# Performance work log

Measured on AMD Instinct MI355X. Metric: run time of the kernel, lower is better.

Reference implementation:

```python
import jax, jax.numpy as jnp
import numpy as np

EPS = 1e-5  # torch BatchNorm default


def setup_inputs() -> dict:
    key = jax.random.key(0)
    ks = jax.random.split(key, 8)
    B, Q, S, C = 4, 256, 128, 256
    feats = [2 * C, 256, 64, 1]  # opt['num_features']
    inp = {
        "support_features": jax.random.normal(ks[0], (B, S, C), dtype=jnp.float32),
        "query_features": jax.random.normal(ks[1], (B, Q, C), dtype=jnp.float32),
    }
    for i in range(3):
        fan_in, fan_out = feats[i], feats[i + 1]
        std = np.sqrt(2.0 / (fan_in + fan_out))  # xavier_normal on conv weight
        inp[f"W{i}"] = jax.random.normal(ks[2 + i], (fan_out, fan_in), dtype=jnp.float32) * std
        inp[f"b{i}"] = jnp.zeros((fan_out,), dtype=jnp.float32)
        inp[f"g{i}"] = jnp.ones((fan_out,), dtype=jnp.float32)   # BN weight
        inp[f"bt{i}"] = jnp.zeros((fan_out,), dtype=jnp.float32)  # BN bias
    return inp


def _bn_relu(x, g, bt):
    # x: [B, N, C]; BatchNorm1d training-mode stats over batch and length dims
    mean = jnp.mean(x, axis=(0, 1))
    var = jnp.mean(jnp.square(x - mean), axis=(0, 1))  # biased var, as torch BN
    return jax.nn.relu((x - mean) * (g * jax.lax.rsqrt(var + EPS)) + bt)


def reference(support_features, query_features,
              W0, b0, g0, bt0, W1, b1, g1, bt1, W2, b2, g2, bt2):
    B, S, C = support_features.shape
    Q = query_features.shape[1]
    # pairwise concat: [B, Q, S, 2C]
    uq = jnp.broadcast_to(query_features[:, :, None, :], (B, Q, S, C))
    us = jnp.broadcast_to(support_features[:, None, :, :], (B, Q, S, C))
    x = jnp.concatenate([uq, us], axis=3).reshape(B, Q * S, 2 * C)
    # 1x1 conv == matmul over channel dim
    x = _bn_relu(jnp.einsum('bnc,oc->bno', x, W0) + b0, g0, bt0)
    x = _bn_relu(jnp.einsum('bnc,oc->bno', x, W1) + b1, g1, bt1)
    x = _bn_relu(jnp.einsum('bnc,oc->bno', x, W2) + b2, g2, bt2)
    # back to [B, C_out, Q, S]
    return jnp.transpose(x, (0, 2, 1)).reshape(B, -1, Q, S)
```

## Files before the change

kernel.cpp:

```cpp
#include <hip/hip_runtime.h>
#include <hip/hip_bf16.h>


typedef __attribute__((ext_vector_type(4))) float f32x4;
typedef __attribute__((ext_vector_type(8))) short s16x8;

#define BN_EPS 1e-5f
#define INV_N  (1.0f/131072.0f)

#define LEAFA(g)   ((g)*16)
#define ROOTA      512
#define GATEA(g)   (528 + (g)*16)
#define CNT_ZERO   1040

__device__ __forceinline__ unsigned pk_bf16(float a, float b) {
  float2 t; t.x = a; t.y = b;
  __hip_bfloat162 h = __float22bfloat162_rn(t);
  return *reinterpret_cast<unsigned*>(&h);
}
__device__ __forceinline__ void split2(float a, float b, unsigned& uh, unsigned& ul) {
  uh = pk_bf16(a, b);
  float ha = __uint_as_float(uh << 16);
  float hb = __uint_as_float(uh & 0xFFFF0000u);
  ul = pk_bf16(a - ha, b - hb);
}

__device__ __forceinline__ unsigned a_ld(const unsigned* p) {
  return __hip_atomic_load(p, __ATOMIC_RELAXED, __HIP_MEMORY_SCOPE_AGENT);
}
__device__ __forceinline__ float a_ldf(const float* p) {
  return __hip_atomic_load(p, __ATOMIC_RELAXED, __HIP_MEMORY_SCOPE_AGENT);
}
__device__ __forceinline__ void a_st(unsigned* p, unsigned v) {
  __hip_atomic_store(p, v, __ATOMIC_RELAXED, __HIP_MEMORY_SCOPE_AGENT);
}
__device__ __forceinline__ void a_stf(float* p, float v) {
  __hip_atomic_store(p, v, __ATOMIC_RELAXED, __HIP_MEMORY_SCOPE_AGENT);
}
__device__ __forceinline__ unsigned a_add(unsigned* p) {
  return __hip_atomic_fetch_add(p, 1u, __ATOMIC_RELAXED, __HIP_MEMORY_SCOPE_AGENT);
}

union frag_u { s16x8 v; unsigned u[4]; };

struct Args {
  const float *Sf, *Qf, *W0, *b0, *g0, *bt0, *W1, *b1, *g1, *bt1, *W2, *b2, *g2, *bt2;
  float *Aq, *As, *y2, *ws0s, *ws1p, *ws1g, *ws1r, *ws2p, *out;
  unsigned *cnt;
};

__global__ __launch_bounds__(64) void k_g0(Args a)
{
  int bi = blockIdx.x, t = threadIdx.x;
  if (bi == 384) {
    for (int i = t; i < CNT_ZERO; i += 64) a.cnt[i] = 0u;
    return;
  }
  int l15 = t & 15, quad = t >> 4;
  int chunk = bi >> 2, ntile = bi & 3;
  bool isQ = (chunk < 64);
  const float* X; float* Out; int m0, koff;
  if (isQ) { m0 = chunk * 16; X = a.Qf; Out = a.Aq; koff = 0; }
  else     { m0 = (chunk - 64) * 16; X = a.Sf; Out = a.As; koff = 256; }
  int n0 = ntile * 64;

  f32x4 acc[4] = {};
#pragma unroll
  for (int ko = 0; ko < 256; ko += 32) {
    const float* row = X + (m0 + l15) * 256 + ko + quad * 8;
    f32x4 v0 = *(const f32x4*)(row);
    f32x4 v1 = *(const f32x4*)(row + 4);
    frag_u ah, al;
#pragma unroll
    for (int j = 0; j < 2; j++) {
      split2(v0[2 * j], v0[2 * j + 1], ah.u[j], al.u[j]);
      split2(v1[2 * j], v1[2 * j + 1], ah.u[2 + j], al.u[2 + j]);
    }
#pragma unroll
    for (int nt = 0; nt < 4; nt++) {
      const float* wrow = a.W0 + (n0 + nt * 16 + l15) * 512 + koff + ko + quad * 8;
      f32x4 w0v = *(const f32x4*)(wrow);
      f32x4 w1v = *(const f32x4*)(wrow + 4);
      frag_u bh, bl;
      split2(w0v[0], w0v[1], bh.u[0], bl.u[0]);
      split2(w0v[2], w0v[3], bh.u[1], bl.u[1]);
      split2(w1v[0], w1v[1], bh.u[2], bl.u[2]);
      split2(w1v[2], w1v[3], bh.u[3], bl.u[3]);
      acc[nt] = __builtin_amdgcn_mfma_f32_16x16x32_bf16(ah.v, bh.v, acc[nt], 0, 0, 0);
      acc[nt] = __builtin_amdgcn_mfma_f32_16x16x32_bf16(al.v, bh.v, acc[nt], 0, 0, 0);
      acc[nt] = __builtin_amdgcn_mfma_f32_16x16x32_bf16(ah.v, bl.v, acc[nt], 0, 0, 0);
    }
  }
#pragma unroll
  for (int nt = 0; nt < 4; nt++) {
    int o = n0 + nt * 16 + l15;
    float bias = isQ ? 0.0f : a.b0[o];
    float cs = 0, cs2 = 0;
#pragma unroll
    for (int r = 0; r < 4; r++) {
      float y = acc[nt][r] + bias;
      Out[(m0 + quad * 4 + r) * 256 + o] = y;
      cs += y; cs2 += y * y;
    }
    cs  += __shfl_xor(cs, 16);  cs  += __shfl_xor(cs, 32);
    cs2 += __shfl_xor(cs2, 16); cs2 += __shfl_xor(cs2, 32);
    if (quad == 0) {
      a.ws0s[chunk * 512 + o] = cs;
      a.ws0s[chunk * 512 + 256 + o] = cs2;
    }
  }
}

__device__ __forceinline__ void bn0_finalize(const Args& a, int t, float* sh_a0c0)
{
  int o = t;
  float sumY = 0, cross = 0, SQ2 = 0, SS2 = 0;
#pragma unroll
  for (int b = 0; b < 4; b++) {
    float sq1 = 0, sq2 = 0, ss1 = 0, ss2 = 0;
#pragma unroll
    for (int c = 0; c < 16; c++) {
      sq1 += a.ws0s[(b * 16 + c) * 512 + o];
      sq2 += a.ws0s[(b * 16 + c) * 512 + 256 + o];
    }
#pragma unroll
    for (int c = 0; c < 8; c++) {
      ss1 += a.ws0s[(64 + b * 8 + c) * 512 + o];
      ss2 += a.ws0s[(64 + b * 8 + c) * 512 + 256 + o];
    }
    SQ2 += sq2; SS2 += ss2;
    sumY += 128.0f * sq1 + 256.0f * ss1;
    cross += sq1 * ss1;
  }
  float mean = sumY * INV_N;
  float var = (128.0f * SQ2 + 256.0f * SS2 + 2.0f * cross) * INV_N - mean * mean;
  float aa = a.g0[o] * rsqrtf(var + BN_EPS);
  sh_a0c0[o] = aa;
  sh_a0c0[256 + o] = a.bt0[o] - mean * aa;
}

__global__ __launch_bounds__(256, 2) void k_f(Args a)
{
  int bi = blockIdx.x, t = threadIdx.x;
  int w = t >> 6, l = t & 63, l15 = l & 15, quad = l >> 4;
  __shared__ ushort w1f[2048 * 8];
  __shared__ float sh_a0c0[512];
  __shared__ float red[2][4][4][16];
  __shared__ float sh_tot[128];
  __shared__ float sh_a1c1[128];
  __shared__ float rs[16], rs2[16];
  __shared__ int s_role;

#pragma unroll
  for (int i = 0; i < 8; i++) {
    int fr = i * 256 + t;
    int kk = fr >> 8, r = fr & 255, nt = r >> 6, ln = r & 63;
    const float* src = a.W1 + (nt * 16 + (ln & 15)) * 256 + kk * 32 + (ln >> 4) * 8;
    f32x4 v0 = *(const f32x4*)(src);
    f32x4 v1 = *(const f32x4*)(src + 4);
    frag_u z;
    z.u[0] = pk_bf16(v0[0], v0[1]); z.u[1] = pk_bf16(v0[2], v0[3]);
    z.u[2] = pk_bf16(v1[0], v1[1]); z.u[3] = pk_bf16(v1[2], v1[3]);
    *(s16x8*)(w1f + fr * 8) = z.v;
  }
  bn0_finalize(a, t, sh_a0c0);
  __syncthreads();

  int b_ = bi >> 7, rem = bi & 127, qt = rem >> 3, st = rem & 7;
  const float* asrow = a.As + ((b_ << 7) + st * 16 + l15) * 256;
  const float* aqrow[4];
#pragma unroll
  for (int mt = 0; mt < 4; mt++)
    aqrow[mt] = a.Aq + ((b_ << 8) + qt * 16 + w * 4 + mt) * 256;

  f32x4 acc[4][4] = {};
#pragma unroll
  for (int kk = 0; kk < 8; kk++) {
    int obase = kk * 32 + quad * 8;
    f32x4 a0v0 = *(const f32x4*)(sh_a0c0 + obase);
    f32x4 a0v1 = *(const f32x4*)(sh_a0c0 + obase + 4);
    f32x4 c0v0 = *(const f32x4*)(sh_a0c0 + 256 + obase);
    f32x4 c0v1 = *(const f32x4*)(sh_a0c0 + 256 + obase + 4);
    f32x4 as0 = *(const f32x4*)(asrow + obase);
    f32x4 as1 = *(const f32x4*)(asrow + obase + 4);

    s16x8 zh[4];
#pragma unroll
    for (int mt = 0; mt < 4; mt++) {
      f32x4 aq0 = *(const f32x4*)(aqrow[mt] + obase);
      f32x4 aq1 = *(const f32x4*)(aqrow[mt] + obase + 4);
      f32x4 z0 = (aq0 + as0) * a0v0 + c0v0;
      f32x4 z1 = (aq1 + as1) * a0v1 + c0v1;
      frag_u zz;
      zz.u[0] = pk_bf16(fmaxf(z0[0], 0.0f), fmaxf(z0[1], 0.0f));
      zz.u[1] = pk_bf16(fmaxf(z0[2], 0.0f), fmaxf(z0[3], 0.0f));
      zz.u[2] = pk_bf16(fmaxf(z1[0], 0.0f), fmaxf(z1[1], 0.0f));
      zz.u[3] = pk_bf16(fmaxf(z1[2], 0.0f), fmaxf(z1[3], 0.0f));
      zh[mt] = zz.v;
    }
#pragma unroll
    for (int nt = 0; nt < 4; nt++) {
      s16x8 bw = *(const s16x8*)(w1f + ((kk * 4 + nt) * 64 + l) * 8);
#pragma unroll
      for (int mt = 0; mt < 4; mt++)
        acc[mt][nt] = __builtin_amdgcn_mfma_f32_16x16x32_bf16(zh[mt], bw, acc[mt][nt], 0, 0, 0);
    }
  }

  float biasv[4];
#pragma unroll
  for (int nt = 0; nt < 4; nt++) biasv[nt] = a.b1[nt * 16 + l15];
  unsigned ku01[4][4], ku23[4][4];
  float s[4] = {0, 0, 0, 0}, s2[4] = {0, 0, 0, 0};
#pragma unroll
  for (int mt = 0; mt < 4; mt++) {
#pragma unroll
    for (int nt = 0; nt < 4; nt++) {
      float y0 = acc[mt][nt][0] + biasv[nt];
      float y1 = acc[mt][nt][1] + biasv[nt];
      float y2v = acc[mt][nt][2] + biasv[nt];
      float y3 = acc[mt][nt][3] + biasv[nt];
      unsigned u01 = pk_bf16(y0, y1), u23 = pk_bf16(y2v, y3);
      ku01[mt][nt] = u01; ku23[mt][nt] = u23;
      float f0 = __uint_as_float(u01 << 16), f1 = __uint_as_float(u01 & 0xFFFF0000u);
      float f2 = __uint_as_float(u23 << 16), f3 = __uint_as_float(u23 & 0xFFFF0000u);
      s[nt]  += f0 + f1 + f2 + f3;
      s2[nt] += f0 * f0 + f1 * f1 + f2 * f2 + f3 * f3;
    }
  }
#pragma unroll
  for (int nt = 0; nt < 4; nt++) {
    float v = s[nt], v2 = s2[nt];
    v  += __shfl_xor(v, 16);  v  += __shfl_xor(v, 32);
    v2 += __shfl_xor(v2, 16); v2 += __shfl_xor(v2, 32);
    if (quad == 0) { red[0][w][nt][l15] = v; red[1][w][nt][l15] = v2; }
  }
  __syncthreads();
  if (t < 128) {
    int which = t >> 6, j = t & 63, nt = j >> 4, jl = j & 15;
    float v = red[which][0][nt][jl] + red[which][1][nt][jl] +
              red[which][2][nt][jl] + red[which][3][nt][jl];
    a_stf(&a.ws1p[bi * 128 + t], v);
  }

  asm volatile("s_waitcnt vmcnt(0)" ::: "memory");
  __syncthreads();
  int g = bi & 31;
  if (t == 0) {
    unsigned old = a_add(&a.cnt[LEAFA(g)]);
    s_role = (old == 15u) ? 1 : 0;
  }
  __syncthreads();
  if (s_role) {
    if (t < 128) {
      float sum = 0;
#pragma unroll
      for (int c = 0; c < 16; c++)
        sum += a_ldf(&a.ws1p[(g + c * 32) * 128 + t]);
      a_stf(&a.ws1g[g * 128 + t], sum);
    }
    asm volatile("s_waitcnt vmcnt(0)" ::: "memory");
    __syncthreads();
    if (t == 0) {
      unsigned r = a_add(&a.cnt[ROOTA]);
      s_role = (r == 31u) ? 2 : 1;
    }
    __syncthreads();
    if (s_role == 2) {
      if (t < 128) {
        float tot = 0;
#pragma unroll
        for (int gg = 0; gg < 32; gg++)
          tot += a_ldf(&a.ws1g[gg * 128 + t]);
        sh_tot[t] = tot;
      }
      __syncthreads();
      if (t < 64) {
        float mean = sh_tot[t] * INV_N;
        float var = sh_tot[64 + t] * INV_N - mean * mean;
        float aa = a.g1[t] * rsqrtf(var + BN_EPS);
        sh_a1c1[t] = aa;
        sh_a1c1[64 + t] = a.bt1[t] - mean * aa;
      }
      __syncthreads();
      if (t < 128) {
        float uv = sh_a1c1[t];
#pragma unroll
        for (int r2 = 0; r2 < 32; r2++)
          a_stf(&a.ws1r[r2 * 128 + t], uv);
      }
      asm volatile("s_waitcnt vmcnt(0)" ::: "memory");
      __syncthreads();
      if (t == 0) {
#pragma unroll
        for (int i = 0; i < 32; i++) a_st(&a.cnt[GATEA(i)], 1u);
      }
    }
  }
  if (t == 0) {
    while (a_ld(&a.cnt[GATEA(g)]) == 0u) __builtin_amdgcn_s_sleep(32);
  }
  __syncthreads();
  if (t < 128)
    sh_a1c1[t] = a_ldf(&a.ws1r[g * 128 + t]);
  __syncthreads();

  float a1v[4], c1v[4], w2v[4];
#pragma unroll
  for (int nt = 0; nt < 4; nt++) {
    int j = nt * 16 + l15;
    a1v[nt] = sh_a1c1[j]; c1v[nt] = sh_a1c1[64 + j]; w2v[nt] = a.W2[j];
  }
  float b2v = a.b2[0];
  float ls = 0, ls2 = 0;
#pragma unroll
  for (int mt = 0; mt < 4; mt++) {
    float part[4] = {0, 0, 0, 0};
#pragma unroll
    for (int nt = 0; nt < 4; nt++) {
      unsigned u01 = ku01[mt][nt], u23 = ku23[mt][nt];
      float f0 = __uint_as_float(u01 << 16), f1 = __uint_as_float(u01 & 0xFFFF0000u);
      float f2 = __uint_as_float(u23 << 16), f3 = __uint_as_float(u23 & 0xFFFF0000u);
      part[0] += fmaxf(a1v[nt] * f0 + c1v[nt], 0.0f) * w2v[nt];
      part[1] += fmaxf(a1v[nt] * f1 + c1v[nt], 0.0f) * w2v[nt];
      part[2] += fmaxf(a1v[nt] * f2 + c1v[nt], 0.0f) * w2v[nt];
      part[3] += fmaxf(a1v[nt] * f3 + c1v[nt], 0.0f) * w2v[nt];
    }
    f32x4 o;
#pragma unroll
    for (int r = 0; r < 4; r++) {
      float pv = part[r];
      pv += __shfl_xor(pv, 1); pv += __shfl_xor(pv, 2);
      pv += __shfl_xor(pv, 4); pv += __shfl_xor(pv, 8);
      float y = pv + b2v;
      o[r] = y;
      if (l15 == 0) { ls += y; ls2 += y * y; }
    }
    if (l15 == 0) {
      int q = qt * 16 + w * 4 + mt;
      int P = ((b_ * 256 + q) * 128) + st * 16 + quad * 4;
      *(f32x4*)(a.y2 + P) = o;
    }
  }
  if (l15 == 0) { rs[t >> 4] = ls; rs2[t >> 4] = ls2; }
  __syncthreads();
  if (t == 0) {
    float sv = 0, sv2 = 0;
#pragma unroll
    for (int i = 0; i < 16; i++) { sv += rs[i]; sv2 += rs2[i]; }
    a.ws2p[bi * 2] = sv;
    a.ws2p[bi * 2 + 1] = sv2;
  }
}

__global__ __launch_bounds__(256) void k_out(Args a)
{
  int t = threadIdx.x;
  __shared__ float wsum[4], wsum2[4];
  __shared__ float fin[2];
  f32x4 v = *(const f32x4*)(a.ws2p + t * 4);
  float s = v[0] + v[2], s2 = v[1] + v[3];
#pragma unroll
  for (int d = 1; d < 64; d <<= 1) { s += __shfl_xor(s, d); s2 += __shfl_xor(s2, d); }
  if ((t & 63) == 0) { wsum[t >> 6] = s; wsum2[t >> 6] = s2; }
  __syncthreads();
  if (t == 0) {
    float sv  = wsum[0] + wsum[1] + wsum[2] + wsum[3];
    float sv2 = wsum2[0] + wsum2[1] + wsum2[2] + wsum2[3];
    float mean = sv * INV_N;
    float var = sv2 * INV_N - mean * mean;
    float aa = a.g2[0] * rsqrtf(var + BN_EPS);
    fin[0] = aa;
    fin[1] = a.bt2[0] - mean * aa;
  }
  __syncthreads();
  float aa = fin[0], cc = fin[1];
  int i = (blockIdx.x * 256 + t) * 4;
  f32x4 y = *(const f32x4*)(a.y2 + i);
  f32x4 o;
#pragma unroll
  for (int r = 0; r < 4; r++) o[r] = fmaxf(aa * y[r] + cc, 0.0f);
  *(f32x4*)(a.out + i) = o;
}

extern "C" void kernel_launch(void* const* d_in, const int* in_sizes, int n_in,
                              void* d_out, int out_size, void* d_ws, size_t ws_size,
                              hipStream_t stream)
{
  float* ws = (float*)d_ws;
  Args a;
  a.Sf  = (const float*)d_in[0];
  a.Qf  = (const float*)d_in[1];
  a.W0  = (const float*)d_in[2];
  a.b0  = (const float*)d_in[3];
  a.g0  = (const float*)d_in[4];
  a.bt0 = (const float*)d_in[5];
  a.W1  = (const float*)d_in[6];
  a.b1  = (const float*)d_in[7];
  a.g1  = (const float*)d_in[8];
  a.bt1 = (const float*)d_in[9];
  a.W2  = (const float*)d_in[10];
  a.b2  = (const float*)d_in[11];
  a.g2  = (const float*)d_in[12];
  a.bt2 = (const float*)d_in[13];

  a.Aq   = ws;
  a.As   = ws + 262144;
  a.y2   = ws + 393216;
  a.ws0s = ws + 524288;
  a.ws1p = ws + 573440;
  a.ws1g = ws + 638976;
  a.ws1r = ws + 643072;
  a.ws2p = ws + 647168;
  a.cnt  = (unsigned*)(ws + 648192);
  a.out  = (float*)d_out;

  k_g0 <<<385, 64, 0, stream>>>(a);
  k_f  <<<512, 256, 0, stream>>>(a);
  k_out<<<128, 256, 0, stream>>>(a);
}
```

Baseline: 123.8 us.

## Finalize BN0 stats once in k_g0 via sentinel spin-wait instead of per-block

```diff
diff --git a/kernel.cpp b/kernel.cpp
--- a/kernel.cpp
+++ b/kernel.cpp
@@ -11,7 +11,11 @@
 #define LEAFA(g)   ((g)*16)
 #define ROOTA      512
 #define GATEA(g)   (528 + (g)*16)
-#define CNT_ZERO   1040
+#define CNT_ZN     1040
+#define ARR0(b)    (1040 + (b)*16)
+#define CNT_TOT    7184
+
+#define SENT 0x9BDF024613572468ull
 
 __device__ __forceinline__ unsigned pk_bf16(float a, float b) {
   float2 t; t.x = a; t.y = b;
@@ -40,31 +44,68 @@
 __device__ __forceinline__ unsigned a_add(unsigned* p) {
   return __hip_atomic_fetch_add(p, 1u, __ATOMIC_RELAXED, __HIP_MEMORY_SCOPE_AGENT);
 }
+__device__ __forceinline__ unsigned long long a_ld64(const unsigned long long* p) {
+  return __hip_atomic_load(p, __ATOMIC_RELAXED, __HIP_MEMORY_SCOPE_AGENT);
+}
+__device__ __forceinline__ void a_st64(unsigned long long* p, unsigned long long v) {
+  __hip_atomic_store(p, v, __ATOMIC_RELAXED, __HIP_MEMORY_SCOPE_AGENT);
+}
 
 union frag_u { s16x8 v; unsigned u[4]; };
 
 struct Args {
   const float *Sf, *Qf, *W0, *b0, *g0, *bt0, *W1, *b1, *g1, *bt1, *W2, *b2, *g2, *bt2;
-  float *Aq, *As, *y2, *ws0s, *ws1p, *ws1g, *ws1r, *ws2p, *out;
+  float *Aq, *As, *y2, *ws0s, *ws1p, *ws1g, *ws1r, *ws2p, *a0c0, *out;
   unsigned *cnt;
 };
 
-__global__ __launch_bounds__(64) void k_g0(Args a)
+__global__ __launch_bounds__(256) void k_g0(Args a)
 {
   int bi = blockIdx.x, t = threadIdx.x;
+  int w = t >> 6, l = t & 63, l15 = l & 15, quad = l >> 4;
+  unsigned long long* C64 = (unsigned long long*)a.cnt;
+
   if (bi == 384) {
-    for (int i = t; i < CNT_ZERO; i += 64) a.cnt[i] = 0u;
+    for (int i = t; i < CNT_ZN; i += 256) a.cnt[i] = 0u;
+    for (int line = t; line < 384; line += 256)
+      while (a_ld64(&C64[ARR0(line) / 2]) != SENT) __builtin_amdgcn_s_sleep(8);
+    __syncthreads();
+    int o = t;
+    float sumY = 0, cross = 0, SQ2 = 0, SS2 = 0;
+#pragma unroll
+    for (int b = 0; b < 4; b++) {
+      float sq1 = 0, sq2 = 0, ss1 = 0, ss2 = 0;
+#pragma unroll
+      for (int c = 0; c < 16; c++) {
+        sq1 += a_ldf(&a.ws0s[(b * 16 + c) * 512 + o]);
+        sq2 += a_ldf(&a.ws0s[(b * 16 + c) * 512 + 256 + o]);
+      }
+#pragma unroll
+      for (int c = 0; c < 8; c++) {
+        ss1 += a_ldf(&a.ws0s[(64 + b * 8 + c) * 512 + o]);
+        ss2 += a_ldf(&a.ws0s[(64 + b * 8 + c) * 512 + 256 + o]);
+      }
+      SQ2 += sq2; SS2 += ss2;
+      sumY += 128.0f * sq1 + 256.0f * ss1;
+      cross += sq1 * ss1;
+    }
+    float mean = sumY * INV_N;
+    float var = (128.0f * SQ2 + 256.0f * SS2 + 2.0f * cross) * INV_N - mean * mean;
+    float aa = a.g0[o] * rsqrtf(var + BN_EPS);
+    a_stf(&a.a0c0[o], aa);
+    a_stf(&a.a0c0[256 + o], a.bt0[o] - mean * aa);
     return;
   }
-  int l15 = t & 15, quad = t >> 4;
-  int chunk = bi >> 2, ntile = bi & 3;
+
+  int gw = bi * 4 + w;
+  int chunk = gw >> 4, nt16 = gw & 15;
   bool isQ = (chunk < 64);
-  const float* X; float* Out; int m0, koff;
-  if (isQ) { m0 = chunk * 16; X = a.Qf; Out = a.Aq; koff = 0; }
-  else     { m0 = (chunk - 64) * 16; X = a.Sf; Out = a.As; koff = 256; }
-  int n0 = ntile * 64;
-
-  f32x4 acc[4] = {};
+  const float* X; float* OutP; int m0, koff;
+  if (isQ) { m0 = chunk * 16; X = a.Qf; OutP = a.Aq; koff = 0; }
+  else     { m0 = (chunk - 64) * 16; X = a.Sf; OutP = a.As; koff = 256; }
+  int o0 = nt16 * 16;
+
+  f32x4 acc0 = {};
 #pragma unroll
   for (int ko = 0; ko < 256; ko += 32) {
     const float* row = X + (m0 + l15) * 256 + ko + quad * 8;
@@ -76,67 +117,36 @@
       split2(v0[2 * j], v0[2 * j + 1], ah.u[j], al.u[j]);
       split2(v1[2 * j], v1[2 * j + 1], ah.u[2 + j], al.u[2 + j]);
     }
-#pragma unroll
-    for (int nt = 0; nt < 4; nt++) {
-      const float* wrow = a.W0 + (n0 + nt * 16 + l15) * 512 + koff + ko + quad * 8;
-      f32x4 w0v = *(const f32x4*)(wrow);
-      f32x4 w1v = *(const f32x4*)(wrow + 4);
-      frag_u bh, bl;
-      split2(w0v[0], w0v[1], bh.u[0], bl.u[0]);
-      split2(w0v[2], w0v[3], bh.u[1], bl.u[1]);
-      split2(w1v[0], w1v[1], bh.u[2], bl.u[2]);
-      split2(w1v[2], w1v[3], bh.u[3], bl.u[3]);
-      acc[nt] = __builtin_amdgcn_mfma_f32_16x16x32_bf16(ah.v, bh.v, acc[nt], 0, 0, 0);
-      acc[nt] = __builtin_amdgcn_mfma_f32_16x16x32_bf16(al.v, bh.v, acc[nt], 0, 0, 0);
-      acc[nt] = __builtin_amdgcn_mfma_f32_16x16x32_bf16(ah.v, bl.v, acc[nt], 0, 0, 0);
-    }
-  }
-#pragma unroll
-  for (int nt = 0; nt < 4; nt++) {
-    int o = n0 + nt * 16 + l15;
-    float bias = isQ ? 0.0f : a.b0[o];
-    float cs = 0, cs2 = 0;
-#pragma unroll
-    for (int r = 0; r < 4; r++) {
-      float y = acc[nt][r] + bias;
-      Out[(m0 + quad * 4 + r) * 256 + o] = y;
-      cs += y; cs2 += y * y;
-    }
-    cs  += __shfl_xor(cs, 16);  cs  += __shfl_xor(cs, 32);
-    cs2 += __shfl_xor(cs2, 16); cs2 += __shfl_xor(cs2, 32);
-    if (quad == 0) {
-      a.ws0s[chunk * 512 + o] = cs;
-      a.ws0s[chunk * 512 + 256 + o] = cs2;
-    }
-  }
-}
-
-__device__ __forceinline__ void bn0_finalize(const Args& a, int t, float* sh_a0c0)
-{
-  int o = t;
-  float sumY = 0, cross = 0, SQ2 = 0, SS2 = 0;
-#pragma unroll
-  for (int b = 0; b < 4; b++) {
-    float sq1 = 0, sq2 = 0, ss1 = 0, ss2 = 0;
-#pragma unroll
-    for (int c = 0; c < 16; c++) {
-      sq1 += a.ws0s[(b * 16 + c) * 512 + o];
-      sq2 += a.ws0s[(b * 16 + c) * 512 + 256 + o];
-    }
-#pragma unroll
-    for (int c = 0; c < 8; c++) {
-      ss1 += a.ws0s[(64 + b * 8 + c) * 512 + o];
-      ss2 += a.ws0s[(64 + b * 8 + c) * 512 + 256 + o];
-    }
-    SQ2 += sq2; SS2 += ss2;
-    sumY += 128.0f * sq1 + 256.0f * ss1;
-    cross += sq1 * ss1;
-  }
-  float mean = sumY * INV_N;
-  float var = (128.0f * SQ2 + 256.0f * SS2 + 2.0f * cross) * INV_N - mean * mean;
-  float aa = a.g0[o] * rsqrtf(var + BN_EPS);
-  sh_a0c0[o] = aa;
-  sh_a0c0[256 + o] = a.bt0[o] - mean * aa;
+    const float* wrow = a.W0 + (o0 + l15) * 512 + koff + ko + quad * 8;
+    f32x4 w0v = *(const f32x4*)(wrow);
+    f32x4 w1v = *(const f32x4*)(wrow + 4);
+    frag_u bh, bl;
+    split2(w0v[0], w0v[1], bh.u[0], bl.u[0]);
+    split2(w0v[2], w0v[3], bh.u[1], bl.u[1]);
+    split2(w1v[0], w1v[1], bh.u[2], bl.u[2]);
+    split2(w1v[2], w1v[3], bh.u[3], bl.u[3]);
+    acc0 = __builtin_amdgcn_mfma_f32_16x16x32_bf16(ah.v, bh.v, acc0, 0, 0, 0);
+    acc0 = __builtin_amdgcn_mfma_f32_16x16x32_bf16(al.v, bh.v, acc0, 0, 0, 0);
+    acc0 = __builtin_amdgcn_mfma_f32_16x16x32_bf16(ah.v, bl.v, acc0, 0, 0, 0);
+  }
+  int o = o0 + l15;
+  float bias = isQ ? 0.0f : a.b0[o];
+  float cs = 0, cs2 = 0;
+#pragma unroll
+  for (int r = 0; r < 4; r++) {
+    float y = acc0[r] + bias;
+    OutP[(m0 + quad * 4 + r) * 256 + o] = y;
+    cs += y; cs2 += y * y;
+  }
+  cs  += __shfl_xor(cs, 16);  cs  += __shfl_xor(cs, 32);
+  cs2 += __shfl_xor(cs2, 16); cs2 += __shfl_xor(cs2, 32);
+  if (quad == 0) {
+    a_stf(&a.ws0s[chunk * 512 + o], cs);
+    a_stf(&a.ws0s[chunk * 512 + 256 + o], cs2);
+  }
+  asm volatile("s_waitcnt vmcnt(0)" ::: "memory");
+  __syncthreads();
+  if (t == 0) a_st64(&C64[ARR0(bi) / 2], SENT);
 }
 
 __global__ __launch_bounds__(256, 2) void k_f(Args a)
@@ -163,7 +173,8 @@
     z.u[2] = pk_bf16(v1[0], v1[1]); z.u[3] = pk_bf16(v1[2], v1[3]);
     *(s16x8*)(w1f + fr * 8) = z.v;
   }
-  bn0_finalize(a, t, sh_a0c0);
+  sh_a0c0[t] = a.a0c0[t];
+  sh_a0c0[256 + t] = a.a0c0[256 + t];
   __syncthreads();
 
   int b_ = bi >> 7, rem = bi & 127, qt = rem >> 3, st = rem & 7;
@@ -412,10 +423,11 @@
   a.ws1g = ws + 638976;
   a.ws1r = ws + 643072;
   a.ws2p = ws + 647168;
-  a.cnt  = (unsigned*)(ws + 648192);
+  a.a0c0 = ws + 648192;
+  a.cnt  = (unsigned*)(ws + 648704);
   a.out  = (float*)d_out;
 
-  k_g0 <<<385, 64, 0, stream>>>(a);
+  k_g0 <<<385, 256, 0, stream>>>(a);
   k_f  <<<512, 256, 0, stream>>>(a);
   k_out<<<128, 256, 0, stream>>>(a);
 }
```

Result: slower. 126.3 us (+2.0%).
